# Optimization experiments

Measured on AMD Instinct MI355X. Metric: run time of the kernel, lower is better.

Reference implementation:

```python
import jax, jax.numpy as jnp
import numpy as np

N_USERS = 100000
M_ITEMS = 50000
EMBED = 64
N_LAYERS = 3
NNZ = 2400000
BATCH = 8192


def setup_inputs() -> dict:
    key = jax.random.key(0)
    ks = jax.random.split(key, 8)
    user = jax.random.randint(ks[0], (BATCH,), 0, N_USERS)
    item_i = jax.random.randint(ks[1], (BATCH,), 0, M_ITEMS)
    item_j = jax.random.randint(ks[2], (BATCH,), 0, M_ITEMS)
    timestamp = jax.random.uniform(ks[3], (BATCH,), dtype=jnp.float32)
    # symmetric bipartite edge list: user->item and item->user halves
    half = NNZ // 2
    u = jax.random.randint(ks[4], (half,), 0, N_USERS)
    it = jax.random.randint(ks[5], (half,), 0, M_ITEMS) + N_USERS
    edge_src = jnp.concatenate([u, it])
    edge_dst = jnp.concatenate([it, u])
    v = jax.random.uniform(ks[6], (half,), dtype=jnp.float32)
    edge_vals = jnp.concatenate([v, v])  # symmetric normalized weights
    embed_user_0 = jax.random.normal(ks[7], (N_USERS, EMBED), dtype=jnp.float32) * 0.1
    embed_item_0 = jax.random.normal(jax.random.fold_in(key, 99), (M_ITEMS, EMBED), dtype=jnp.float32) * 0.1
    return {
        'user': user, 'item_i': item_i, 'item_j': item_j,
        'timestamp': timestamp, 'split_idx': 0,
        'edge_src': edge_src, 'edge_dst': edge_dst, 'edge_vals': edge_vals,
        'embed_user_0': embed_user_0, 'embed_item_0': embed_item_0,
    }


def reference(user, item_i, item_j, timestamp, split_idx,
              edge_src, edge_dst, edge_vals, embed_user_0, embed_item_0):
    N = N_USERS + M_ITEMS
    # LightGCN propagation: mean over layer-0..n_layers embeddings
    all_emb = jnp.concatenate([embed_user_0, embed_item_0], axis=0)  # [N, D]
    emb = all_emb
    emb_sum = all_emb
    for _ in range(N_LAYERS):
        # sparse.mm(Graph, emb): gather source features along edges, scale, segment-reduce
        emb = jax.ops.segment_sum(edge_vals[:, None] * emb[edge_dst], edge_src,
                                  num_segments=N)
        emb_sum = emb_sum + emb
    light_out = emb_sum / (N_LAYERS + 1)
    embed_user = light_out[:N_USERS]
    embed_item = light_out[N_USERS:]

    ue = embed_user[user]          # [B, D]
    ie = embed_item[item_i]        # [B, D]
    je = embed_item[item_j]        # [B, D]
    prediction_i = jnp.sum(ue * ie, axis=-1)
    prediction_j = jnp.sum(ue * je, axis=-1)

    # reg_loss uses layer-0 embeddings gathered at the batch indices
    u0 = embed_user_0[user]
    i0 = embed_item_0[item_i]
    j0 = embed_item_0[item_j]
    reg_loss = 0.5 * (jnp.sum(u0 * u0) + jnp.sum(i0 * i0) + jnp.sum(j0 * j0)) / user.shape[0]
    return prediction_i, prediction_j, reg_loss
```

## Files before the change

### kernel.cpp

```cpp
#include <hip/hip_runtime.h>

#define N_USERS 100000
#define M_ITEMS 50000
#define NNODES  (N_USERS + M_ITEMS)
#define EMBED   64
#define N_LAYERS 3
#define BATCH   8192

#define NU_E ((size_t)N_USERS * EMBED)
#define NI_E ((size_t)M_ITEMS * EMBED)
#define NE   ((size_t)NNODES * EMBED)

#define NPB    256
#define NBUCK  ((NNODES + NPB - 1) / NPB)
#define PBLK   256
#define HBB_N  (NBUCK * PBLK)
#define SCAN_NB ((HBB_N + 1023) / 1024)
#define PRED_BLOCKS ((BATCH * 64) / 256)

typedef unsigned int uint;

static __device__ __forceinline__ ushort f2bf(float f) {
    uint u = __float_as_uint(f);
    return (ushort)((u + 0x7fffu + ((u >> 16) & 1u)) >> 16);
}
static __device__ __forceinline__ float bf_lo(uint u) { return __uint_as_float(u << 16); }
static __device__ __forceinline__ float bf_hi(uint u) { return __uint_as_float(u & 0xffff0000u); }
static __device__ __forceinline__ float bfs(ushort u) { return __uint_as_float((uint)u << 16); }

__global__ void init_and_hist(const float* __restrict__ eu, const float* __restrict__ ei,
                              ushort* __restrict__ E0,
                              const int* __restrict__ src, int* __restrict__ Hbb,
                              int nnz, int tile) {
    __shared__ int h[NBUCK];
    if (blockIdx.x < PBLK) {
        for (int i = threadIdx.x; i < NBUCK; i += blockDim.x) h[i] = 0;
        __syncthreads();
        int base = blockIdx.x * tile;
        int end  = min(base + tile, nnz);
        for (int i = base + threadIdx.x; i < end; i += blockDim.x)
            atomicAdd(&h[src[i] >> 8], 1);
        __syncthreads();
        for (int i = threadIdx.x; i < NBUCK; i += blockDim.x)
            Hbb[i * PBLK + blockIdx.x] = h[i];
    } else {
        size_t t = (size_t)(blockIdx.x - PBLK) * blockDim.x + threadIdx.x;
        const size_t nu4 = NU_E / 4;
        const size_t n4  = NE / 4;
        if (t >= n4) return;
        float4 v = (t < nu4) ? ((const float4*)eu)[t] : ((const float4*)ei)[t - nu4];
        ((ushort4*)E0)[t] = make_ushort4(f2bf(v.x), f2bf(v.y), f2bf(v.z), f2bf(v.w));
    }
}

__global__ void scan_local(int* __restrict__ h, int* __restrict__ bsum, int n) {
    __shared__ int lds[256];
    const int tid = threadIdx.x;
    const int base = blockIdx.x * 1024 + tid * 4;
    int v[4]; int s = 0;
    #pragma unroll
    for (int c = 0; c < 4; ++c) { v[c] = (base + c < n) ? h[base + c] : 0; s += v[c]; }
    lds[tid] = s;
    __syncthreads();
    for (int off = 1; off < 256; off <<= 1) {
        int t = (tid >= off) ? lds[tid - off] : 0;
        __syncthreads();
        lds[tid] += t;
        __syncthreads();
    }
    if (tid == 255) bsum[blockIdx.x] = lds[255];
    int run = (tid > 0) ? lds[tid - 1] : 0;
    #pragma unroll
    for (int c = 0; c < 4; ++c) {
        int t = v[c];
        if (base + c < n) h[base + c] = run;
        run += t;
    }
}

__global__ void scan_add2(int* __restrict__ h, const int* __restrict__ bsum,
                          int n, int nblk) {
    __shared__ int lds[256];
    int tid = threadIdx.x;
    if (tid < 256) lds[tid] = (tid < nblk) ? bsum[tid] : 0;
    __syncthreads();
    for (int off = 1; off < 256; off <<= 1) {
        int t = (tid >= off && tid < 256) ? lds[tid - off] : 0;
        __syncthreads();
        if (tid < 256) lds[tid] += t;
        __syncthreads();
    }
    int prefix = (blockIdx.x > 0) ? lds[blockIdx.x - 1] : 0;
    int i = blockIdx.x * 1024 + tid;
    if (i < n) h[i] += prefix;
}

__global__ void partition2(const int* __restrict__ src, const int* __restrict__ dst,
                           const float* __restrict__ vals, const int* __restrict__ Hbb,
                           int2* __restrict__ ebuf, int nnz, int tile) {
    __shared__ int cur[NBUCK];
    for (int i = threadIdx.x; i < NBUCK; i += blockDim.x)
        cur[i] = Hbb[i * PBLK + blockIdx.x];
    __syncthreads();
    int base = blockIdx.x * tile;
    int end  = min(base + tile, nnz);
    for (int i = base + threadIdx.x; i < end; i += blockDim.x) {
        int s = src[i];
        int d = dst[i];
        float v = vals[i];
        if (d >= N_USERS) d -= N_USERS;
        int p = atomicAdd(&cur[s >> 8], 1);
        ebuf[p] = make_int2((s & 255) | (d << 8), __float_as_int(v));
    }
}

__global__ void bucket_sort_perm(const int* __restrict__ Hbb, const int2* __restrict__ ebuf,
                                 int* __restrict__ offs, int2* __restrict__ ep,
                                 int* __restrict__ perm, int nnz) {
    __shared__ int cnt[256];
    __shared__ int sc[256];
    __shared__ int cur[256];
    __shared__ int dsc[256];
    int b   = blockIdx.x;
    int tid = threadIdx.x;
    int beg = Hbb[b * PBLK];
    int end = (b + 1 < NBUCK) ? Hbb[(b + 1) * PBLK] : nnz;
    if (tid < 256) cnt[tid] = 0;
    __syncthreads();
    for (int i = beg + tid; i < end; i += blockDim.x)
        atomicAdd(&cnt[ebuf[i].x & 255], 1);
    __syncthreads();
    if (tid < 256) sc[tid] = cnt[tid];
    __syncthreads();
    for (int off = 1; off < 256; off <<= 1) {
        int t = (tid >= off && tid < 256) ? sc[tid - off] : 0;
        __syncthreads();
        if (tid < 256) sc[tid] += t;
        __syncthreads();
    }
    if (tid < 256) {
        int nodeBase = beg + ((tid > 0) ? sc[tid - 1] : 0);
        int node = b * NPB + tid;
        if (node < NNODES) offs[node] = nodeBase;
        cur[tid] = nodeBase;
    }
    __syncthreads();
    for (int i = beg + tid; i < end; i += blockDim.x) {
        int2 e = ebuf[i];
        int p = atomicAdd(&cur[e.x & 255], 1);
        ep[p] = make_int2(e.x >> 8, e.y);
    }
    __syncthreads();
    if (tid < 256) sc[tid] = 0;
    __syncthreads();
    int nodeCount = min(NNODES - b * NPB, NPB);
    int deg = 0;
    if (tid < nodeCount) {
        deg = min(cnt[tid], 255);
        atomicAdd(&sc[deg], 1);
    }
    __syncthreads();
    if (tid < 256) dsc[tid] = sc[tid];
    __syncthreads();
    for (int off = 1; off < 256; off <<= 1) {
        int t = (tid >= off && tid < 256) ? dsc[tid - off] : 0;
        __syncthreads();
        if (tid < 256) dsc[tid] += t;
        __syncthreads();
    }
    if (tid < 256) cur[tid] = b * NPB + ((tid > 0) ? dsc[tid - 1] : 0);
    __syncthreads();
    if (tid < nodeCount) {
        int rank = atomicAdd(&cur[deg], 1);
        perm[rank] = b * NPB + tid;
    }
    if (b == 0 && tid == 0) offs[NNODES] = nnz;
}

__global__ void gather_E(const int* __restrict__ offs, const int2* __restrict__ ep,
                         const int* __restrict__ perm,
                         const ushort* __restrict__ Eprev, ushort* __restrict__ Enext,
                         int nnz) {
    int t = blockIdx.x * blockDim.x + threadIdx.x;
    int wave = t >> 6;
    int lane = t & 63;
    int g = lane >> 3;
    int q = lane & 7;
    int ln = wave * 8 + g;
    bool valid = ln < NNODES;
    int node = valid ? perm[ln] : 0;
    int start = valid ? offs[node] : 0;
    int deg   = valid ? offs[node + 1] - start : 0;
    bool isUser = node < N_USERS;
    const uint4* other = (const uint4*)(Eprev + (isUser ? NU_E : 0));
    int lastIdx = min(max(start + deg - 1, 0), nnz - 1);

    int md = deg;
    #pragma unroll
    for (int off = 8; off <= 32; off <<= 1) md = max(md, __shfl_xor(md, off));

    float a0=0.f,a1=0.f,a2=0.f,a3=0.f,a4=0.f,a5=0.f,a6=0.f,a7=0.f;
    for (int k = 0; k < md; k += 8) {
        int2 e[8];
        uint4 r[8];
        #pragma unroll
        for (int c = 0; c < 8; ++c) {
            int idx = (k + c < deg) ? start + k + c : lastIdx;
            e[c] = ep[idx];
            if (k + c >= deg) e[c].y = 0;
        }
        #pragma unroll
        for (int c = 0; c < 8; ++c)
            r[c] = other[(size_t)e[c].x * 8 + q];
        #pragma unroll
        for (int c = 0; c < 8; ++c) {
            float v = __int_as_float(e[c].y);
            a0 = fmaf(v, bf_lo(r[c].x), a0);  a1 = fmaf(v, bf_hi(r[c].x), a1);
            a2 = fmaf(v, bf_lo(r[c].y), a2);  a3 = fmaf(v, bf_hi(r[c].y), a3);
            a4 = fmaf(v, bf_lo(r[c].z), a4);  a5 = fmaf(v, bf_hi(r[c].z), a5);
            a6 = fmaf(v, bf_lo(r[c].w), a6);  a7 = fmaf(v, bf_hi(r[c].w), a7);
        }
    }

    if (!valid) return;
    uint4 o;
    o.x = (uint)f2bf(a0) | ((uint)f2bf(a1) << 16);
    o.y = (uint)f2bf(a2) | ((uint)f2bf(a3) << 16);
    o.z = (uint)f2bf(a4) | ((uint)f2bf(a5) << 16);
    o.w = (uint)f2bf(a6) | ((uint)f2bf(a7) << 16);
    ((uint4*)Enext)[(size_t)node * 8 + q] = o;
}

__global__ void predict_kernel(const int* __restrict__ user, const int* __restrict__ item_i,
                               const int* __restrict__ item_j,
                               const ushort* __restrict__ E0, const ushort* __restrict__ E1,
                               const ushort* __restrict__ E2, const ushort* __restrict__ E3,
                               const float* __restrict__ eu0, const float* __restrict__ ei0,
                               float* __restrict__ out, float* __restrict__ rbuf) {
    __shared__ float rpart[4];
    int t = blockIdx.x * blockDim.x + threadIdx.x;
    int b = t >> 6;
    int d = t & 63;
    int wv = threadIdx.x >> 6;
    float pi = 0.f, pj = 0.f, r = 0.f;
    if (b < BATCH) {
        size_t ru = (size_t)user[b] * EMBED + d;
        size_t ri = ((size_t)N_USERS + item_i[b]) * EMBED + d;
        size_t rj = ((size_t)N_USERS + item_j[b]) * EMBED + d;
        float ue = bfs(E0[ru]) + bfs(E1[ru]) + bfs(E2[ru]) + bfs(E3[ru]);
        float ie = bfs(E0[ri]) + bfs(E1[ri]) + bfs(E2[ri]) + bfs(E3[ri]);
        float je = bfs(E0[rj]) + bfs(E1[rj]) + bfs(E2[rj]) + bfs(E3[rj]);
        pi = ue * ie;
        pj = ue * je;
        float u0 = eu0[(size_t)user[b] * EMBED + d];
        float i0 = ei0[(size_t)item_i[b] * EMBED + d];
        float j0 = ei0[(size_t)item_j[b] * EMBED + d];
        r = u0 * u0 + i0 * i0 + j0 * j0;
    }
    #pragma unroll
    for (int off = 32; off > 0; off >>= 1) {
        pi += __shfl_down(pi, off);
        pj += __shfl_down(pj, off);
        r  += __shfl_down(r,  off);
    }
    if (d == 0 && b < BATCH) {
        out[b]         = pi * (1.0f / 16.0f);
        out[BATCH + b] = pj * (1.0f / 16.0f);
        rpart[wv] = r;
    }
    __syncthreads();
    if (threadIdx.x == 0)
        rbuf[blockIdx.x] = rpart[0] + rpart[1] + rpart[2] + rpart[3];
}

__global__ void finalize_reg(const float* __restrict__ rbuf, float* __restrict__ out) {
    __shared__ float lds[4];
    int tid = threadIdx.x;
    float s = 0.f;
    for (int i = tid; i < PRED_BLOCKS; i += 256) s += rbuf[i];
    #pragma unroll
    for (int off = 32; off > 0; off >>= 1) s += __shfl_down(s, off);
    if ((tid & 63) == 0) lds[tid >> 6] = s;
    __syncthreads();
    if (tid == 0)
        out[2 * BATCH] = (lds[0] + lds[1] + lds[2] + lds[3]) * (0.5f / (float)BATCH);
}

extern "C" void kernel_launch(void* const* d_in, const int* in_sizes, int n_in,
                              void* d_out, int out_size, void* d_ws, size_t ws_size,
                              hipStream_t stream) {
    const int*   user      = (const int*)  d_in[0];
    const int*   item_i    = (const int*)  d_in[1];
    const int*   item_j    = (const int*)  d_in[2];
    const int*   edge_src  = (const int*)  d_in[5];
    const int*   edge_dst  = (const int*)  d_in[6];
    const float* edge_vals = (const float*)d_in[7];
    const float* eu0       = (const float*)d_in[8];
    const float* ei0       = (const float*)d_in[9];
    const int    nnz       = in_sizes[5];

    float* out = (float*)d_out;

    ushort* E0   = (ushort*)d_ws;
    ushort* E1   = E0 + NE;
    ushort* E2   = E1 + NE;
    ushort* E3   = E2 + NE;
    int2*   ep   = (int2*)(E3 + NE);
    int*    offs = (int*)(ep + nnz);
    int*    Hbb  = offs + NNODES + 2;
    int*    bsum = Hbb + HBB_N;
    int*    perm = bsum + 256;
    float*  rbuf = (float*)(perm + NNODES);
    int2*   ebuf = (int2*)E1;

    const int tile = (nnz + PBLK - 1) / PBLK;
    const int initBlocks = (int)((NE / 4 + 1023) / 1024);

    init_and_hist<<<PBLK + initBlocks, 1024, 0, stream>>>(
        eu0, ei0, E0, edge_src, Hbb, nnz, tile);
    scan_local<<<SCAN_NB, 256, 0, stream>>>(Hbb, bsum, HBB_N);
    scan_add2<<<SCAN_NB, 1024, 0, stream>>>(Hbb, bsum, HBB_N, SCAN_NB);
    partition2<<<PBLK, 1024, 0, stream>>>(edge_src, edge_dst, edge_vals,
                                          Hbb, ebuf, nnz, tile);
    bucket_sort_perm<<<NBUCK, 1024, 0, stream>>>(Hbb, ebuf, offs, ep, perm, nnz);
    const int gblocks = (int)((((NNODES + 7) / 8) * 64 + 255) / 256);
    gather_E<<<gblocks, 256, 0, stream>>>(offs, ep, perm, E0, E1, nnz);
    gather_E<<<gblocks, 256, 0, stream>>>(offs, ep, perm, E1, E2, nnz);
    gather_E<<<gblocks, 256, 0, stream>>>(offs, ep, perm, E2, E3, nnz);
    predict_kernel<<<PRED_BLOCKS, 256, 0, stream>>>(
        user, item_i, item_j, E0, E1, E2, E3, eu0, ei0, out, rbuf);
    finalize_reg<<<1, 256, 0, stream>>>(rbuf, out);
}
```

Before: 334.5 us.

## Fuse CSR build phases into one cooperative kernel with grid syncs

Replaces the five CSR-construction kernels (histogram, two-level scan, partition, per-bucket sort) with a single cooperative kernel of 256 blocks that separates the phases with grid.sync(). The bf16 conversion of the initial embeddings moves into the tail of this kernel as a grid-stride loop. The degree-sorted permutation is also reversed so that nodes are ordered by descending degree. This removes launch gaps between small kernels, but the per-bucket sort now runs on only 256 blocks instead of NBUCK blocks, which may serialize that phase.

```diff
diff --git a/kernel.cpp b/kernel.cpp
--- a/kernel.cpp
+++ b/kernel.cpp
@@ -1,21 +1,22 @@
 #include <hip/hip_runtime.h>
+#include <hip/hip_cooperative_groups.h>
+
+namespace cg = cooperative_groups;
 
 #define N_USERS 100000
 #define M_ITEMS 50000
 #define NNODES  (N_USERS + M_ITEMS)
 #define EMBED   64
-#define N_LAYERS 3
 #define BATCH   8192
 
 #define NU_E ((size_t)N_USERS * EMBED)
-#define NI_E ((size_t)M_ITEMS * EMBED)
 #define NE   ((size_t)NNODES * EMBED)
 
 #define NPB    256
 #define NBUCK  ((NNODES + NPB - 1) / NPB)
 #define PBLK   256
 #define HBB_N  (NBUCK * PBLK)
-#define SCAN_NB ((HBB_N + 1023) / 1024)
+#define CH     (HBB_N / PBLK)
 #define PRED_BLOCKS ((BATCH * 64) / 256)
 
 typedef unsigned int uint;
@@ -28,153 +29,143 @@
 static __device__ __forceinline__ float bf_hi(uint u) { return __uint_as_float(u & 0xffff0000u); }
 static __device__ __forceinline__ float bfs(ushort u) { return __uint_as_float((uint)u << 16); }
 
-__global__ void init_and_hist(const float* __restrict__ eu, const float* __restrict__ ei,
-                              ushort* __restrict__ E0,
-                              const int* __restrict__ src, int* __restrict__ Hbb,
-                              int nnz, int tile) {
-    __shared__ int h[NBUCK];
-    if (blockIdx.x < PBLK) {
-        for (int i = threadIdx.x; i < NBUCK; i += blockDim.x) h[i] = 0;
-        __syncthreads();
-        int base = blockIdx.x * tile;
-        int end  = min(base + tile, nnz);
-        for (int i = base + threadIdx.x; i < end; i += blockDim.x)
-            atomicAdd(&h[src[i] >> 8], 1);
-        __syncthreads();
-        for (int i = threadIdx.x; i < NBUCK; i += blockDim.x)
-            Hbb[i * PBLK + blockIdx.x] = h[i];
-    } else {
-        size_t t = (size_t)(blockIdx.x - PBLK) * blockDim.x + threadIdx.x;
-        const size_t nu4 = NU_E / 4;
-        const size_t n4  = NE / 4;
-        if (t >= n4) return;
-        float4 v = (t < nu4) ? ((const float4*)eu)[t] : ((const float4*)ei)[t - nu4];
-        ((ushort4*)E0)[t] = make_ushort4(f2bf(v.x), f2bf(v.y), f2bf(v.z), f2bf(v.w));
-    }
-}
-
-__global__ void scan_local(int* __restrict__ h, int* __restrict__ bsum, int n) {
-    __shared__ int lds[256];
+__global__ void csr_build(const float* __restrict__ eu, const float* __restrict__ ei,
+                          ushort* __restrict__ E0,
+                          const int* __restrict__ src, const int* __restrict__ dst,
+                          const float* __restrict__ vals,
+                          int* __restrict__ Hbb, int* __restrict__ bsum,
+                          int2* __restrict__ ebuf,
+                          int* __restrict__ offs, int2* __restrict__ ep,
+                          int* __restrict__ perm, int nnz, int tile) {
+    cg::grid_group grid = cg::this_grid();
+    __shared__ int h[1024];
+    __shared__ int cnt[256], sc2[256], cur2[256], dsc[256];
+    const int blk = blockIdx.x;
     const int tid = threadIdx.x;
-    const int base = blockIdx.x * 1024 + tid * 4;
-    int v[4]; int s = 0;
-    #pragma unroll
-    for (int c = 0; c < 4; ++c) { v[c] = (base + c < n) ? h[base + c] : 0; s += v[c]; }
-    lds[tid] = s;
-    __syncthreads();
-    for (int off = 1; off < 256; off <<= 1) {
-        int t = (tid >= off) ? lds[tid - off] : 0;
-        __syncthreads();
-        lds[tid] += t;
-        __syncthreads();
-    }
-    if (tid == 255) bsum[blockIdx.x] = lds[255];
-    int run = (tid > 0) ? lds[tid - 1] : 0;
-    #pragma unroll
-    for (int c = 0; c < 4; ++c) {
-        int t = v[c];
-        if (base + c < n) h[base + c] = run;
-        run += t;
-    }
-}
-
-__global__ void scan_add2(int* __restrict__ h, const int* __restrict__ bsum,
-                          int n, int nblk) {
-    __shared__ int lds[256];
-    int tid = threadIdx.x;
-    if (tid < 256) lds[tid] = (tid < nblk) ? bsum[tid] : 0;
-    __syncthreads();
-    for (int off = 1; off < 256; off <<= 1) {
-        int t = (tid >= off && tid < 256) ? lds[tid - off] : 0;
-        __syncthreads();
-        if (tid < 256) lds[tid] += t;
-        __syncthreads();
-    }
-    int prefix = (blockIdx.x > 0) ? lds[blockIdx.x - 1] : 0;
-    int i = blockIdx.x * 1024 + tid;
-    if (i < n) h[i] += prefix;
-}
-
-__global__ void partition2(const int* __restrict__ src, const int* __restrict__ dst,
-                           const float* __restrict__ vals, const int* __restrict__ Hbb,
-                           int2* __restrict__ ebuf, int nnz, int tile) {
-    __shared__ int cur[NBUCK];
-    for (int i = threadIdx.x; i < NBUCK; i += blockDim.x)
-        cur[i] = Hbb[i * PBLK + blockIdx.x];
-    __syncthreads();
-    int base = blockIdx.x * tile;
-    int end  = min(base + tile, nnz);
-    for (int i = base + threadIdx.x; i < end; i += blockDim.x) {
+    const int base = blk * tile;
+    const int end  = min(base + tile, nnz);
+
+    for (int i = tid; i < NBUCK; i += 1024) h[i] = 0;
+    __syncthreads();
+    for (int i = base + tid; i < end; i += 1024)
+        atomicAdd(&h[src[i] >> 8], 1);
+    __syncthreads();
+    for (int i = tid; i < NBUCK; i += 1024)
+        Hbb[i * PBLK + blk] = h[i];
+    grid.sync();
+
+    {
+        int v = (tid < CH) ? Hbb[blk * CH + tid] : 0;
+        h[tid] = v;
+        __syncthreads();
+        for (int off = 1; off < 1024; off <<= 1) {
+            int t = (tid >= off) ? h[tid - off] : 0;
+            __syncthreads();
+            h[tid] += t;
+            __syncthreads();
+        }
+        if (tid == 1023) bsum[blk] = h[1023];
+        if (tid < CH) Hbb[blk * CH + tid] = (tid > 0) ? h[tid - 1] : 0;
+    }
+    grid.sync();
+
+    if (blk == 0) {
+        int v = (tid < PBLK) ? bsum[tid] : 0;
+        h[tid] = v;
+        __syncthreads();
+        for (int off = 1; off < 256; off <<= 1) {
+            int t = (tid >= off && tid < 256) ? h[tid - off] : 0;
+            __syncthreads();
+            if (tid < 256) h[tid] += t;
+            __syncthreads();
+        }
+        if (tid < PBLK) bsum[tid] = (tid > 0) ? h[tid - 1] : 0;
+    }
+    grid.sync();
+
+    {
+        int prefix = bsum[blk];
+        if (tid < CH) Hbb[blk * CH + tid] += prefix;
+    }
+    grid.sync();
+
+    for (int i = tid; i < NBUCK; i += 1024) h[i] = Hbb[i * PBLK + blk];
+    __syncthreads();
+    for (int i = base + tid; i < end; i += 1024) {
         int s = src[i];
         int d = dst[i];
         float v = vals[i];
         if (d >= N_USERS) d -= N_USERS;
-        int p = atomicAdd(&cur[s >> 8], 1);
+        int p = atomicAdd(&h[s >> 8], 1);
         ebuf[p] = make_int2((s & 255) | (d << 8), __float_as_int(v));
     }
-}
-
-__global__ void bucket_sort_perm(const int* __restrict__ Hbb, const int2* __restrict__ ebuf,
-                                 int* __restrict__ offs, int2* __restrict__ ep,
-                                 int* __restrict__ perm, int nnz) {
-    __shared__ int cnt[256];
-    __shared__ int sc[256];
-    __shared__ int cur[256];
-    __shared__ int dsc[256];
-    int b   = blockIdx.x;
-    int tid = threadIdx.x;
-    int beg = Hbb[b * PBLK];
-    int end = (b + 1 < NBUCK) ? Hbb[(b + 1) * PBLK] : nnz;
-    if (tid < 256) cnt[tid] = 0;
-    __syncthreads();
-    for (int i = beg + tid; i < end; i += blockDim.x)
-        atomicAdd(&cnt[ebuf[i].x & 255], 1);
-    __syncthreads();
-    if (tid < 256) sc[tid] = cnt[tid];
-    __syncthreads();
-    for (int off = 1; off < 256; off <<= 1) {
-        int t = (tid >= off && tid < 256) ? sc[tid - off] : 0;
-        __syncthreads();
-        if (tid < 256) sc[tid] += t;
-        __syncthreads();
-    }
-    if (tid < 256) {
-        int nodeBase = beg + ((tid > 0) ? sc[tid - 1] : 0);
-        int node = b * NPB + tid;
-        if (node < NNODES) offs[node] = nodeBase;
-        cur[tid] = nodeBase;
-    }
-    __syncthreads();
-    for (int i = beg + tid; i < end; i += blockDim.x) {
-        int2 e = ebuf[i];
-        int p = atomicAdd(&cur[e.x & 255], 1);
-        ep[p] = make_int2(e.x >> 8, e.y);
-    }
-    __syncthreads();
-    if (tid < 256) sc[tid] = 0;
-    __syncthreads();
-    int nodeCount = min(NNODES - b * NPB, NPB);
-    int deg = 0;
-    if (tid < nodeCount) {
-        deg = min(cnt[tid], 255);
-        atomicAdd(&sc[deg], 1);
-    }
-    __syncthreads();
-    if (tid < 256) dsc[tid] = sc[tid];
-    __syncthreads();
-    for (int off = 1; off < 256; off <<= 1) {
-        int t = (tid >= off && tid < 256) ? dsc[tid - off] : 0;
-        __syncthreads();
-        if (tid < 256) dsc[tid] += t;
-        __syncthreads();
-    }
-    if (tid < 256) cur[tid] = b * NPB + ((tid > 0) ? dsc[tid - 1] : 0);
-    __syncthreads();
-    if (tid < nodeCount) {
-        int rank = atomicAdd(&cur[deg], 1);
-        perm[rank] = b * NPB + tid;
-    }
-    if (b == 0 && tid == 0) offs[NNODES] = nnz;
+    grid.sync();
+
+    for (int b = blk; b < NBUCK; b += PBLK) {
+        int bbeg = Hbb[b * PBLK];
+        int bend = (b + 1 < NBUCK) ? Hbb[(b + 1) * PBLK] : nnz;
+        __syncthreads();
+        if (tid < 256) cnt[tid] = 0;
+        __syncthreads();
+        for (int i = bbeg + tid; i < bend; i += 1024)
+            atomicAdd(&cnt[ebuf[i].x & 255], 1);
+        __syncthreads();
+        if (tid < 256) sc2[tid] = cnt[tid];
+        __syncthreads();
+        for (int off = 1; off < 256; off <<= 1) {
+            int t = (tid >= off && tid < 256) ? sc2[tid - off] : 0;
+            __syncthreads();
+            if (tid < 256) sc2[tid] += t;
+            __syncthreads();
+        }
+        if (tid < 256) {
+            int nodeBase = bbeg + ((tid > 0) ? sc2[tid - 1] : 0);
+            int node = b * NPB + tid;
+            if (node < NNODES) offs[node] = nodeBase;
+            cur2[tid] = nodeBase;
+        }
+        __syncthreads();
+        for (int i = bbeg + tid; i < bend; i += 1024) {
+            int2 e = ebuf[i];
+            int p = atomicAdd(&cur2[e.x & 255], 1);
+            ep[p] = make_int2(e.x >> 8, e.y);
+        }
+        __syncthreads();
+        if (tid < 256) sc2[tid] = 0;
+        __syncthreads();
+        int nodeCount = min(NNODES - b * NPB, NPB);
+        int bin = 0;
+        if (tid < nodeCount) {
+            bin = 255 - min(cnt[tid], 255);
+            atomicAdd(&sc2[bin], 1);
+        }
+        __syncthreads();
+        if (tid < 256) dsc[tid] = sc2[tid];
+        __syncthreads();
+        for (int off = 1; off < 256; off <<= 1) {
+            int t = (tid >= off && tid < 256) ? dsc[tid - off] : 0;
+            __syncthreads();
+            if (tid < 256) dsc[tid] += t;
+            __syncthreads();
+        }
+        if (tid < 256) cur2[tid] = b * NPB + ((tid > 0) ? dsc[tid - 1] : 0);
+        __syncthreads();
+        if (tid < nodeCount) {
+            int rank = atomicAdd(&cur2[bin], 1);
+            perm[rank] = b * NPB + tid;
+        }
+    }
+    if (blk == 0 && tid == 0) offs[NNODES] = nnz;
+
+    {
+        const size_t nu4 = NU_E / 4;
+        const size_t n4  = NE / 4;
+        for (size_t t4 = (size_t)blk * 1024 + tid; t4 < n4; t4 += (size_t)PBLK * 1024) {
+            float4 v = (t4 < nu4) ? ((const float4*)eu)[t4]
+                                  : ((const float4*)ei)[t4 - nu4];
+            ((ushort4*)E0)[t4] = make_ushort4(f2bf(v.x), f2bf(v.y), f2bf(v.z), f2bf(v.w));
+        }
+    }
 }
 
 __global__ void gather_E(const int* __restrict__ offs, const int2* __restrict__ ep,
@@ -297,7 +288,7 @@
     const float* edge_vals = (const float*)d_in[7];
     const float* eu0       = (const float*)d_in[8];
     const float* ei0       = (const float*)d_in[9];
-    const int    nnz       = in_sizes[5];
+    int          nnz       = in_sizes[5];
 
     float* out = (float*)d_out;
 
@@ -313,20 +304,23 @@
     float*  rbuf = (float*)(perm + NNODES);
     int2*   ebuf = (int2*)E1;
 
-    const int tile = (nnz + PBLK - 1) / PBLK;
-    const int initBlocks = (int)((NE / 4 + 1023) / 1024);
-
-    init_and_hist<<<PBLK + initBlocks, 1024, 0, stream>>>(
-        eu0, ei0, E0, edge_src, Hbb, nnz, tile);
-    scan_local<<<SCAN_NB, 256, 0, stream>>>(Hbb, bsum, HBB_N);
-    scan_add2<<<SCAN_NB, 1024, 0, stream>>>(Hbb, bsum, HBB_N, SCAN_NB);
-    partition2<<<PBLK, 1024, 0, stream>>>(edge_src, edge_dst, edge_vals,
-                                          Hbb, ebuf, nnz, tile);
-    bucket_sort_perm<<<NBUCK, 1024, 0, stream>>>(Hbb, ebuf, offs, ep, perm, nnz);
+    int tile = (nnz + PBLK - 1) / PBLK;
+
+    void* cargs[] = {
+        (void*)&eu0, (void*)&ei0, (void*)&E0,
+        (void*)&edge_src, (void*)&edge_dst, (void*)&edge_vals,
+        (void*)&Hbb, (void*)&bsum, (void*)&ebuf,
+        (void*)&offs, (void*)&ep, (void*)&perm,
+        (void*)&nnz, (void*)&tile
+    };
+    hipLaunchCooperativeKernel((const void*)csr_build, dim3(PBLK), dim3(1024),
+                               cargs, 0, stream);
+
     const int gblocks = (int)((((NNODES + 7) / 8) * 64 + 255) / 256);
     gather_E<<<gblocks, 256, 0, stream>>>(offs, ep, perm, E0, E1, nnz);
     gather_E<<<gblocks, 256, 0, stream>>>(offs, ep, perm, E1, E2, nnz);
     gather_E<<<gblocks, 256, 0, stream>>>(offs, ep, perm, E2, E3, nnz);
+
     predict_kernel<<<PRED_BLOCKS, 256, 0, stream>>>(
         user, item_i, item_j, E0, E1, E2, E3, eu0, ei0, out, rbuf);
     finalize_reg<<<1, 256, 0, stream>>>(rbuf, out);
```

Result: slower. 507.8 us (+51.8%).

## Stage edge partition and bucket sort through LDS for coalesced global writes

Applied to the files above, without the earlier changes.

The partition kernel now processes its tile in LDS-sized chunks. It builds a per-chunk histogram and scan, scatters edges into shared memory, then copies each bucket's run to global memory contiguously using 16-lane groups. The bucket sort likewise scatters into an LDS buffer when the bucket fits and writes the result back coalesced, falling back to direct global scatter otherwise. Node permutation order within a bucket is flipped to descending degree. All of this aims to replace random global scatter writes with coalesced ones, at the cost of more barriers, a 1024-wide scan, and large LDS use that limits occupancy.

```diff
diff --git a/kernel.cpp b/kernel.cpp
--- a/kernel.cpp
+++ b/kernel.cpp
@@ -4,11 +4,9 @@
 #define M_ITEMS 50000
 #define NNODES  (N_USERS + M_ITEMS)
 #define EMBED   64
-#define N_LAYERS 3
 #define BATCH   8192
 
 #define NU_E ((size_t)N_USERS * EMBED)
-#define NI_E ((size_t)M_ITEMS * EMBED)
 #define NE   ((size_t)NNODES * EMBED)
 
 #define NPB    256
@@ -16,6 +14,8 @@
 #define PBLK   256
 #define HBB_N  (NBUCK * PBLK)
 #define SCAN_NB ((HBB_N + 1023) / 1024)
+#define PTILE  4688
+#define BCAP   6784
 #define PRED_BLOCKS ((BATCH * 64) / 256)
 
 typedef unsigned int uint;
@@ -95,39 +95,77 @@
     if (i < n) h[i] += prefix;
 }
 
-__global__ void partition2(const int* __restrict__ src, const int* __restrict__ dst,
-                           const float* __restrict__ vals, const int* __restrict__ Hbb,
-                           int2* __restrict__ ebuf, int nnz, int tile) {
-    __shared__ int cur[NBUCK];
-    for (int i = threadIdx.x; i < NBUCK; i += blockDim.x)
-        cur[i] = Hbb[i * PBLK + blockIdx.x];
-    __syncthreads();
-    int base = blockIdx.x * tile;
-    int end  = min(base + tile, nnz);
-    for (int i = base + threadIdx.x; i < end; i += blockDim.x) {
-        int s = src[i];
-        int d = dst[i];
-        float v = vals[i];
-        if (d >= N_USERS) d -= N_USERS;
-        int p = atomicAdd(&cur[s >> 8], 1);
-        ebuf[p] = make_int2((s & 255) | (d << 8), __float_as_int(v));
-    }
-}
-
-__global__ void bucket_sort_perm(const int* __restrict__ Hbb, const int2* __restrict__ ebuf,
-                                 int* __restrict__ offs, int2* __restrict__ ep,
-                                 int* __restrict__ perm, int nnz) {
-    __shared__ int cnt[256];
-    __shared__ int sc[256];
-    __shared__ int cur[256];
-    __shared__ int dsc[256];
+__global__ void __launch_bounds__(1024)
+partition2(const int* __restrict__ src, const int* __restrict__ dst,
+           const float* __restrict__ vals, const int* __restrict__ Hbb,
+           int2* __restrict__ ebuf, int nnz, int tile) {
+    __shared__ int2 data[PTILE];
+    __shared__ int  cnt[NBUCK];
+    __shared__ int  cur[NBUCK];
+    __shared__ int  gcur[NBUCK];
+    __shared__ int  s[1024];
+    const int blk = blockIdx.x;
+    const int tid = threadIdx.x;
+    const int base = blk * tile;
+    const int end  = min(base + tile, nnz);
+
+    for (int i = tid; i < NBUCK; i += 1024) gcur[i] = Hbb[i * PBLK + blk];
+    __syncthreads();
+
+    for (int h0 = base; h0 < end; h0 += PTILE) {
+        int h1 = min(h0 + PTILE, end);
+        for (int i = tid; i < NBUCK; i += 1024) cnt[i] = 0;
+        __syncthreads();
+        for (int i = h0 + tid; i < h1; i += 1024)
+            atomicAdd(&cnt[src[i] >> 8], 1);
+        __syncthreads();
+        s[tid] = (tid < NBUCK) ? cnt[tid] : 0;
+        __syncthreads();
+        for (int off = 1; off < 1024; off <<= 1) {
+            int t = (tid >= off) ? s[tid - off] : 0;
+            __syncthreads();
+            s[tid] += t;
+            __syncthreads();
+        }
+        if (tid < NBUCK) cur[tid] = (tid > 0) ? s[tid - 1] : 0;
+        __syncthreads();
+        for (int i = h0 + tid; i < h1; i += 1024) {
+            int sv = src[i];
+            int d  = dst[i];
+            float v = vals[i];
+            if (d >= N_USERS) d -= N_USERS;
+            int p = atomicAdd(&cur[sv >> 8], 1);
+            data[p] = make_int2((sv & 255) | (d << 8), __float_as_int(v));
+        }
+        __syncthreads();
+        int grp = tid >> 4, lane16 = tid & 15;
+        for (int b = grp; b < NBUCK; b += 64) {
+            int lbeg = (b > 0) ? s[b - 1] : 0;
+            int c  = cnt[b];
+            int gb = gcur[b];
+            for (int j = lane16; j < c; j += 16)
+                ebuf[gb + j] = data[lbeg + j];
+        }
+        __syncthreads();
+        if (tid < NBUCK) gcur[tid] += cnt[tid];
+        __syncthreads();
+    }
+}
+
+__global__ void __launch_bounds__(1024)
+bucket_sort_perm(const int* __restrict__ Hbb, const int2* __restrict__ ebuf,
+                 int* __restrict__ offs, int2* __restrict__ ep,
+                 int* __restrict__ perm, int nnz) {
+    __shared__ int2 data[BCAP];
+    __shared__ int cnt[256], sc[256], cur[256], dsc[256];
     int b   = blockIdx.x;
     int tid = threadIdx.x;
     int beg = Hbb[b * PBLK];
     int end = (b + 1 < NBUCK) ? Hbb[(b + 1) * PBLK] : nnz;
+    int blen = end - beg;
     if (tid < 256) cnt[tid] = 0;
     __syncthreads();
-    for (int i = beg + tid; i < end; i += blockDim.x)
+    for (int i = beg + tid; i < end; i += 1024)
         atomicAdd(&cnt[ebuf[i].x & 255], 1);
     __syncthreads();
     if (tid < 256) sc[tid] = cnt[tid];
@@ -139,25 +177,36 @@
         __syncthreads();
     }
     if (tid < 256) {
-        int nodeBase = beg + ((tid > 0) ? sc[tid - 1] : 0);
+        int lbase = (tid > 0) ? sc[tid - 1] : 0;
         int node = b * NPB + tid;
-        if (node < NNODES) offs[node] = nodeBase;
-        cur[tid] = nodeBase;
-    }
-    __syncthreads();
-    for (int i = beg + tid; i < end; i += blockDim.x) {
-        int2 e = ebuf[i];
-        int p = atomicAdd(&cur[e.x & 255], 1);
-        ep[p] = make_int2(e.x >> 8, e.y);
+        if (node < NNODES) offs[node] = beg + lbase;
+        cur[tid] = lbase;
+    }
+    __syncthreads();
+    if (blen <= BCAP) {
+        for (int i = beg + tid; i < end; i += 1024) {
+            int2 e = ebuf[i];
+            int p = atomicAdd(&cur[e.x & 255], 1);
+            data[p] = make_int2(e.x >> 8, e.y);
+        }
+        __syncthreads();
+        for (int i = tid; i < blen; i += 1024)
+            ep[beg + i] = data[i];
+    } else {
+        for (int i = beg + tid; i < end; i += 1024) {
+            int2 e = ebuf[i];
+            int p = atomicAdd(&cur[e.x & 255], 1);
+            ep[beg + p] = make_int2(e.x >> 8, e.y);
+        }
     }
     __syncthreads();
     if (tid < 256) sc[tid] = 0;
     __syncthreads();
     int nodeCount = min(NNODES - b * NPB, NPB);
-    int deg = 0;
+    int bin = 0;
     if (tid < nodeCount) {
-        deg = min(cnt[tid], 255);
-        atomicAdd(&sc[deg], 1);
+        bin = 255 - min(cnt[tid], 255);
+        atomicAdd(&sc[bin], 1);
     }
     __syncthreads();
     if (tid < 256) dsc[tid] = sc[tid];
@@ -171,7 +220,7 @@
     if (tid < 256) cur[tid] = b * NPB + ((tid > 0) ? dsc[tid - 1] : 0);
     __syncthreads();
     if (tid < nodeCount) {
-        int rank = atomicAdd(&cur[deg], 1);
+        int rank = atomicAdd(&cur[bin], 1);
         perm[rank] = b * NPB + tid;
     }
     if (b == 0 && tid == 0) offs[NNODES] = nnz;
```

Measured after the change: 320.8 us. 1.04x faster.
